# Performance work log

Hardware: AMD Instinct MI355X
Metric: run time of the kernel (lower is better)

Reference implementation:

```python
import jax, jax.numpy as jnp
import numpy as np

HIDDEN_DIM = 256
NLAT, NLON = 64, 128
BATCH, N_STATIONS = 2, 1024


def _grid_coords():
    lat = jnp.linspace(-90.0, 90.0, NLAT)
    lon = jnp.linspace(-180.0, 180.0, NLON)
    lat_mesh, lon_mesh = jnp.meshgrid(lat, lon, indexing='ij')
    return lat_mesh.reshape(-1), lon_mesh.reshape(-1)  # (n_grid,)


def setup_inputs() -> dict:
    key = jax.random.key(0)
    k1, k2, k3, k4, k5, k6 = jax.random.split(key, 6)
    station_features = jax.random.normal(k1, (BATCH, N_STATIONS, HIDDEN_DIM), dtype=jnp.float32)
    station_coords = jax.random.normal(k2, (BATCH, N_STATIONS, 3), dtype=jnp.float32)
    mask = jnp.ones((BATCH, N_STATIONS), dtype=jnp.float32)
    # distance_mlp params: Linear(3,32) -> GELU -> Linear(32,1) -> Softplus
    W1 = jax.random.normal(k3, (3, 32), dtype=jnp.float32) * (1.0 / np.sqrt(3.0))
    b1 = jax.random.normal(k4, (32,), dtype=jnp.float32) * 0.02
    W2 = jax.random.normal(k5, (32, 1), dtype=jnp.float32) * (1.0 / np.sqrt(32.0))
    b2 = jax.random.normal(k6, (1,), dtype=jnp.float32) * 0.02
    return {"station_features": station_features, "station_coords": station_coords,
            "mask": mask, "W1": W1, "b1": b1, "W2": W2, "b2": b2}


def reference(station_features, station_coords, mask, W1, b1, W2, b2):
    lat_grid, lon_grid = _grid_coords()  # (G,)
    station_lat = station_coords[:, :, 0]  # (B,S)
    station_lon = station_coords[:, :, 1]
    dlat = station_lat[:, :, None] - lat_grid[None, None, :]  # (B,S,G)
    dlon = station_lon[:, :, None] - lon_grid[None, None, :]
    dist = jnp.sqrt(dlat**2 + dlon**2 + 1e-6)
    dist_features = jnp.stack([dist, dlat, dlon], axis=-1)  # (B,S,G,3)
    h = jax.nn.gelu(dist_features @ W1 + b1, approximate=False)  # (B,S,G,32)
    weights = jax.nn.softplus((h @ W2 + b2)[..., 0])  # (B,S,G)
    weights = weights * mask[:, :, None]
    weights = jax.nn.softmax(weights, axis=1)  # over stations
    grid = jnp.einsum('bsg,bsd->bgd', weights, station_features)
    grid = grid.reshape(station_features.shape[0], NLAT, NLON, HIDDEN_DIM)
    return jnp.transpose(grid, (0, 3, 1, 2))  # (B, D, nlat, nlon)
```

## Files before the change

kernel.cpp:

```cpp
#include <hip/hip_runtime.h>
#include <math.h>

#define NLAT 64
#define NLON 128
#define HID  256
#define NSTA 1024
#define NG   (NLAT * NLON)
#define TG   16
#define SC   128
#define NCH  4
#define NGRP 16
#define TABN 2048
#define TABW 4.5f

#define LOG2E 1.4426950408889634f
#define LN2   0.69314718055994531f

typedef float f32x4 __attribute__((ext_vector_type(4)));
typedef _Float16 f16x8 __attribute__((ext_vector_type(8)));

__device__ __forceinline__ float gelu_ref(float x) {
    const float p  = 0.3275911f;
    const float a1 = 0.254829592f, a2 = -0.284496736f, a3 = 1.421413741f,
                a4 = -1.453152027f, a5 = 1.061405429f;
    float z  = x * 0.70710678118654752f;
    float az = fabsf(z);
    float t  = __builtin_amdgcn_rcpf(fmaf(p, az, 1.0f));
    float poly = fmaf(fmaf(fmaf(fmaf(a5, t, a4), t, a3), t, a2), t, a1) * t;
    float e  = __builtin_amdgcn_exp2f(az * az * -LOG2E);
    float r  = fmaf(-poly, e, 1.0f);
    float erfz = copysignf(r, z);
    float hx = 0.5f * x;
    return fmaf(hx, erfz, hx);
}

__global__ __launch_bounds__(256)
void cvt_kernel(const float* __restrict__ feats, _Float16* __restrict__ fhi,
                _Float16* __restrict__ flo) {
    __shared__ float tile[32][68];
    const int blk = blockIdx.x;
    const int b  = blk >> 7;
    const int st = (blk >> 2) & 31;
    const int dt = blk & 3;
    {
        const int s  = threadIdx.x >> 3;
        const int dq = threadIdx.x & 7;
        const float* src = feats + ((size_t)(b * NSTA + st * 32 + s)) * HID + dt * 64 + dq * 8;
        float4 v0 = *(const float4*)src;
        float4 v1 = *(const float4*)(src + 4);
        *(float4*)&tile[s][dq * 8]     = v0;
        *(float4*)&tile[s][dq * 8 + 4] = v1;
    }
    __syncthreads();
    const int d  = threadIdx.x >> 2;
    const int sq = threadIdx.x & 3;
    f16x8 hi8, lo8;
#pragma unroll
    for (int k = 0; k < 8; ++k) {
        float v = tile[sq * 8 + k][d];
        _Float16 h = (_Float16)v;
        hi8[k] = h;
        lo8[k] = (_Float16)(v - (float)h);
    }
    const size_t o = ((size_t)(b * HID + dt * 64 + d)) * NSTA + st * 32 + sq * 8;
    *(f16x8*)&fhi[o] = hi8;
    *(f16x8*)&flo[o] = lo8;
}

__global__ __launch_bounds__(256, 6)
void s2g_kernel(const float* __restrict__ coords,
                const float* __restrict__ maskp,
                const float* __restrict__ W1,
                const float* __restrict__ b1,
                const float* __restrict__ W2,
                const float* __restrict__ b2p,
                const _Float16* __restrict__ fhi,
                const _Float16* __restrict__ flo,
                float* __restrict__ out,
                float* __restrict__ acc1,
                float2* __restrict__ ml)
{
    __shared__ float gtab[TABN];
    __shared__ __align__(16) f16x8 fragAh[256];
    __shared__ __align__(16) f16x8 fragAl[256];
    __shared__ __align__(16) float slat[SC], slon[SC], smask[SC];
    __shared__ float4 wpack[32];
    __shared__ float2 w2pk[32];
    __shared__ __align__(16) float redbuf[NGRP * TG];
    __shared__ __align__(16) float mS[TG], lS[TG], alphaS[TG];

    const int tid  = threadIdx.x;
    const int half = blockIdx.x >> 10;
    const int b    = (blockIdx.x >> 9) & 1;
    const int blk  = blockIdx.x & 511;
    const int lat  = blk >> 3;
    const int lon0 = (blk & 7) * TG;
    const int sbase = half * (NSTA / 2);

    const float latv = -90.0f + (180.0f / 63.0f) * (float)lat;

    const float CELL   = TABW / (float)TABN;
    const float ISCALE = (float)TABN / TABW;

#pragma unroll
    for (int k = tid; k < TABN; k += 256) {
        float x = ((float)k + 0.5f) * CELL;
        gtab[k] = gelu_ref(-x);
    }
    if (tid < 32) {
        wpack[tid] = make_float4(W1[tid] * ISCALE, W1[32 + tid] * ISCALE,
                                 W1[64 + tid] * ISCALE, b1[tid] * ISCALE);
        w2pk[tid]  = make_float2(W2[tid], W2[tid] * CELL);
        if (tid < TG) { mS[tid] = -1.0e30f; lS[tid] = 0.0f; }
    }
    const float b2 = b2p[0];

    const int gA   = tid & (TG - 1);
    const int sgrp = tid >> 4;
    const float lonvA = -180.0f + (360.0f / 127.0f) * (float)(lon0 + gA);

    const int lane = tid & 63;
    const int wv   = tid >> 6;

    f32x4 acc[4];
#pragma unroll
    for (int t = 0; t < 4; ++t) acc[t] = (f32x4){0.0f, 0.0f, 0.0f, 0.0f};

    const float* cbase = coords + (size_t)b * NSTA * 3;
    const float* mbase = maskp  + (size_t)b * NSTA;
    const _Float16* fhb = fhi + (size_t)b * HID * NSTA;
    const _Float16* flb = flo + (size_t)b * HID * NSTA;

    for (int c = 0; c < NCH; ++c) {
        const int s0 = sbase + c * SC;
        __syncthreads();
        if (tid < SC) {
            slat[tid]  = cbase[(size_t)(s0 + tid) * 3 + 0];
            slon[tid]  = cbase[(size_t)(s0 + tid) * 3 + 1];
            smask[tid] = mbase[s0 + tid];
        }
        __syncthreads();

        float dist[8], dlat[8], dlon[8], v[8];
#pragma unroll
        for (int i = 0; i < 8; ++i) {
            int s = sgrp * 8 + i;
            float dla = slat[s] - latv;
            float dlo = slon[s] - lonvA;
            dlat[i] = dla;
            dlon[i] = dlo;
            dist[i] = sqrtf(fmaf(dla, dla, fmaf(dlo, dlo, 1e-6f)));
            v[i] = b2;
        }
#pragma unroll 2
        for (int j = 0; j < 32; ++j) {
            float4 wj = wpack[j];
            float2 w2 = w2pk[j];
#pragma unroll
            for (int i = 0; i < 8; ++i) {
                float pre = fmaf(wj.x, dist[i], fmaf(wj.y, dlat[i], fmaf(wj.z, dlon[i], wj.w)));
                float a   = fminf(fabsf(pre), (float)TABN - 0.5f);
                int  idx  = (int)a;
                float r   = gtab[idx];
                v[i] = fmaf(w2.y, fmaxf(pre, 0.0f), v[i]);
                v[i] = fmaf(w2.x, r, v[i]);
            }
        }
        float lmax = -3.0e38f;
#pragma unroll
        for (int i = 0; i < 8; ++i) {
            int s = sgrp * 8 + i;
            float x  = v[i];
            float ax = fabsf(x);
            float e  = __builtin_amdgcn_exp2f(-ax * LOG2E);
            float sp = fmaxf(x, 0.0f) + __builtin_amdgcn_logf(1.0f + e) * LN2;
            v[i] = sp * smask[s];
            lmax = fmaxf(lmax, v[i]);
        }
        redbuf[sgrp * TG + gA] = lmax;
        __syncthreads();

        if (tid < TG) {
            float cm = redbuf[tid];
#pragma unroll
            for (int k = 1; k < NGRP; ++k) cm = fmaxf(cm, redbuf[k * TG + tid]);
            float mold = mS[tid];
            float mnew = fmaxf(mold, cm);
            alphaS[tid] = __builtin_amdgcn_exp2f((mold - mnew) * LOG2E);
            mS[tid] = mnew;
        }
        __syncthreads();

        {
            float m  = mS[gA];
            float ps = 0.0f;
            f16x8 fh, fl;
#pragma unroll
            for (int i = 0; i < 8; ++i) {
                float p = __builtin_amdgcn_exp2f((v[i] - m) * LOG2E);
                _Float16 h = (_Float16)p;
                fh[i] = h;
                fl[i] = (_Float16)(p - (float)h);
                ps += p;
            }
            const int idx = ((sgrp >> 2) << 6) + (((sgrp & 3) << 4) | gA);
            fragAh[idx] = fh;
            fragAl[idx] = fl;
            redbuf[sgrp * TG + gA] = ps;
        }
        __syncthreads();

        if (tid < TG) {
            float t = 0.0f;
#pragma unroll
            for (int k = 0; k < NGRP; ++k) t += redbuf[k * TG + tid];
            lS[tid] = lS[tid] * alphaS[tid] + t;
        }

        {
            const f32x4 al = *(const f32x4*)&alphaS[(lane >> 4) * 4];
#pragma unroll
            for (int t = 0; t < 4; ++t) acc[t] = acc[t] * al;

            const int srow = s0 + ((lane >> 4) * 8);
            const int dbase = wv * 64 + (lane & 15);
#pragma unroll
            for (int kc = 0; kc < 4; ++kc) {
                f16x8 ah = fragAh[(kc << 6) + lane];
                f16x8 al16 = fragAl[(kc << 6) + lane];
#pragma unroll
                for (int t = 0; t < 4; ++t) {
                    const size_t off = (size_t)(dbase + t * 16) * NSTA + srow + kc * 32;
                    f16x8 bh = *(const f16x8*)(fhb + off);
                    f16x8 bl = *(const f16x8*)(flb + off);
                    acc[t] = __builtin_amdgcn_mfma_f32_16x16x32_f16(ah, bh, acc[t], 0, 0, 0);
                    acc[t] = __builtin_amdgcn_mfma_f32_16x16x32_f16(ah, bl, acc[t], 0, 0, 0);
                    acc[t] = __builtin_amdgcn_mfma_f32_16x16x32_f16(al16, bh, acc[t], 0, 0, 0);
                }
            }
        }
    }
    __syncthreads();

    {
        float* dst = half ? acc1 : out;
        const int m0 = (lane >> 4) * 4;
        const size_t gbase = (size_t)lat * NLON + lon0 + m0;
#pragma unroll
        for (int t = 0; t < 4; ++t) {
            const int d = wv * 64 + t * 16 + (lane & 15);
            *reinterpret_cast<f32x4*>(dst + ((size_t)(b * HID + d)) * NG + gbase) = acc[t];
        }
        if (tid < TG)
            ml[((half << 1) + b) * NG + lat * NLON + lon0 + tid] = make_float2(mS[tid], lS[tid]);
    }
}

__global__ __launch_bounds__(256)
void comb_kernel(float* __restrict__ out, const float* __restrict__ acc1,
                 const float2* __restrict__ ml) {
    const int x    = blockIdx.x;
    const int b    = x >> 9;
    const int lat  = (x >> 3) & 63;
    const int dseg = x & 7;
    const int lon  = threadIdx.x & 127;
    const int dsub = threadIdx.x >> 7;
    const int g    = lat * NLON + lon;

    const float2 p0 = ml[b * NG + g];
    const float2 p1 = ml[(2 + b) * NG + g];
    const float M  = fmaxf(p0.x, p1.x);
    float s0 = __builtin_amdgcn_exp2f((p0.x - M) * LOG2E);
    float s1 = __builtin_amdgcn_exp2f((p1.x - M) * LOG2E);
    const float rl = 1.0f / fmaf(p0.y, s0, p1.y * s1);
    s0 *= rl; s1 *= rl;

#pragma unroll 4
    for (int k = 0; k < 16; ++k) {
        const int d = dseg * 32 + dsub + k * 2;
        const size_t o = ((size_t)(b * HID + d)) * NG + g;
        out[o] = fmaf(out[o], s0, acc1[o] * s1);
    }
}

extern "C" void kernel_launch(void* const* d_in, const int* in_sizes, int n_in,
                              void* d_out, int out_size, void* d_ws, size_t ws_size,
                              hipStream_t stream) {
    const float* feats  = (const float*)d_in[0];
    const float* coords = (const float*)d_in[1];
    const float* maskp  = (const float*)d_in[2];
    const float* W1     = (const float*)d_in[3];
    const float* b1     = (const float*)d_in[4];
    const float* W2     = (const float*)d_in[5];
    const float* b2     = (const float*)d_in[6];
    float* out          = (float*)d_out;

    _Float16* fhi = (_Float16*)d_ws;
    _Float16* flo = fhi + (size_t)2 * HID * NSTA;
    float*  acc1 = (float*)((char*)d_ws + (size_t)2 * 1048576);
    float2* ml   = (float2*)((char*)d_ws + (size_t)2 * 1048576 + (size_t)2 * HID * NG * 4);

    hipLaunchKernelGGL(cvt_kernel, dim3(256), dim3(256), 0, stream, feats, fhi, flo);
    hipLaunchKernelGGL(s2g_kernel, dim3(2048), dim3(256), 0, stream,
                       coords, maskp, W1, b1, W2, b2, fhi, flo, out, acc1, ml);
    hipLaunchKernelGGL(comb_kernel, dim3(1024), dim3(256), 0, stream, out, acc1, ml);
}
```

Measured before the change: 255.0 us.

## Fold GELU linear part into per-station term and precompute weights in prep kernel

```diff
diff --git a/kernel.cpp b/kernel.cpp
--- a/kernel.cpp
+++ b/kernel.cpp
@@ -35,10 +35,37 @@
 }
 
 __global__ __launch_bounds__(256)
-void cvt_kernel(const float* __restrict__ feats, _Float16* __restrict__ fhi,
-                _Float16* __restrict__ flo) {
+void cvt_kernel(const float* __restrict__ feats,
+                const float* __restrict__ W1, const float* __restrict__ b1,
+                const float* __restrict__ W2, const float* __restrict__ b2p,
+                _Float16* __restrict__ fhi, _Float16* __restrict__ flo,
+                float* __restrict__ wbuf) {
+    const int blk = blockIdx.x;
+    if (blk == 256) {
+        if (threadIdx.x == 0) {
+            const float ISCALE = (float)TABN / TABW;
+            const float CELL   = TABW / (float)TABN;
+            float A = 0.0f, B = 0.0f, C = 0.0f, D = b2p[0];
+            for (int j = 0; j < 32; ++j) {
+                float a = W1[j], b = W1[32 + j], c = W1[64 + j], d = b1[j], w2 = W2[j];
+                wbuf[j * 8 + 0] = a * ISCALE;
+                wbuf[j * 8 + 1] = b * ISCALE;
+                wbuf[j * 8 + 2] = c * ISCALE;
+                wbuf[j * 8 + 3] = d * ISCALE;
+                wbuf[j * 8 + 4] = w2;
+                wbuf[j * 8 + 5] = 0.5f * w2 * CELL;
+                wbuf[j * 8 + 6] = 0.0f;
+                wbuf[j * 8 + 7] = 0.0f;
+                A = fmaf(0.5f * w2, a, A);
+                B = fmaf(0.5f * w2, b, B);
+                C = fmaf(0.5f * w2, c, C);
+                D = fmaf(0.5f * w2, d, D);
+            }
+            wbuf[256] = A; wbuf[257] = B; wbuf[258] = C; wbuf[259] = D;
+        }
+        return;
+    }
     __shared__ float tile[32][68];
-    const int blk = blockIdx.x;
     const int b  = blk >> 7;
     const int st = (blk >> 2) & 31;
     const int dt = blk & 3;
@@ -70,10 +97,7 @@
 __global__ __launch_bounds__(256, 6)
 void s2g_kernel(const float* __restrict__ coords,
                 const float* __restrict__ maskp,
-                const float* __restrict__ W1,
-                const float* __restrict__ b1,
-                const float* __restrict__ W2,
-                const float* __restrict__ b2p,
+                const float* __restrict__ wbuf,
                 const _Float16* __restrict__ fhi,
                 const _Float16* __restrict__ flo,
                 float* __restrict__ out,
@@ -83,10 +107,8 @@
     __shared__ float gtab[TABN];
     __shared__ __align__(16) f16x8 fragAh[256];
     __shared__ __align__(16) f16x8 fragAl[256];
-    __shared__ __align__(16) float slat[SC], slon[SC], smask[SC];
-    __shared__ float4 wpack[32];
-    __shared__ float2 w2pk[32];
-    __shared__ __align__(16) float redbuf[NGRP * TG];
+    __shared__ __align__(16) float maxbuf[NGRP * TG];
+    __shared__ __align__(16) float psum[NGRP * TG];
     __shared__ __align__(16) float mS[TG], lS[TG], alphaS[TG];
 
     const int tid  = threadIdx.x;
@@ -98,22 +120,17 @@
     const int sbase = half * (NSTA / 2);
 
     const float latv = -90.0f + (180.0f / 63.0f) * (float)lat;
-
-    const float CELL   = TABW / (float)TABN;
-    const float ISCALE = (float)TABN / TABW;
-
+    const float LIM  = (float)TABN - 0.5f;
+
+    const float CELL = TABW / (float)TABN;
 #pragma unroll
     for (int k = tid; k < TABN; k += 256) {
         float x = ((float)k + 0.5f) * CELL;
         gtab[k] = gelu_ref(-x);
     }
-    if (tid < 32) {
-        wpack[tid] = make_float4(W1[tid] * ISCALE, W1[32 + tid] * ISCALE,
-                                 W1[64 + tid] * ISCALE, b1[tid] * ISCALE);
-        w2pk[tid]  = make_float2(W2[tid], W2[tid] * CELL);
-        if (tid < TG) { mS[tid] = -1.0e30f; lS[tid] = 0.0f; }
-    }
-    const float b2 = b2p[0];
+    if (tid < TG) { mS[tid] = -1.0e30f; lS[tid] = 0.0f; }
+
+    const f32x4 lin = *(const f32x4*)&wbuf[256];
 
     const int gA   = tid & (TG - 1);
     const int sgrp = tid >> 4;
@@ -131,59 +148,55 @@
     const _Float16* fhb = fhi + (size_t)b * HID * NSTA;
     const _Float16* flb = flo + (size_t)b * HID * NSTA;
 
+    __syncthreads();
+
     for (int c = 0; c < NCH; ++c) {
         const int s0 = sbase + c * SC;
-        __syncthreads();
-        if (tid < SC) {
-            slat[tid]  = cbase[(size_t)(s0 + tid) * 3 + 0];
-            slon[tid]  = cbase[(size_t)(s0 + tid) * 3 + 1];
-            smask[tid] = mbase[s0 + tid];
-        }
-        __syncthreads();
 
         float dist[8], dlat[8], dlon[8], v[8];
 #pragma unroll
         for (int i = 0; i < 8; ++i) {
-            int s = sgrp * 8 + i;
-            float dla = slat[s] - latv;
-            float dlo = slon[s] - lonvA;
+            const int s = s0 + sgrp * 8 + i;
+            float sla = cbase[(size_t)s * 3 + 0];
+            float slo = cbase[(size_t)s * 3 + 1];
+            float dla = sla - latv;
+            float dlo = slo - lonvA;
             dlat[i] = dla;
             dlon[i] = dlo;
-            dist[i] = sqrtf(fmaf(dla, dla, fmaf(dlo, dlo, 1e-6f)));
-            v[i] = b2;
+            float dss = sqrtf(fmaf(dla, dla, fmaf(dlo, dlo, 1e-6f)));
+            dist[i] = dss;
+            v[i] = fmaf(lin.x, dss, fmaf(lin.y, dla, fmaf(lin.z, dlo, lin.w)));
         }
 #pragma unroll 2
         for (int j = 0; j < 32; ++j) {
-            float4 wj = wpack[j];
-            float2 w2 = w2pk[j];
+            const f32x4 wq = *(const f32x4*)&wbuf[j * 8];
+            const float2 wp = *(const float2*)&wbuf[j * 8 + 4];
 #pragma unroll
             for (int i = 0; i < 8; ++i) {
-                float pre = fmaf(wj.x, dist[i], fmaf(wj.y, dlat[i], fmaf(wj.z, dlon[i], wj.w)));
-                float a   = fminf(fabsf(pre), (float)TABN - 0.5f);
-                int  idx  = (int)a;
-                float r   = gtab[idx];
-                v[i] = fmaf(w2.y, fmaxf(pre, 0.0f), v[i]);
-                v[i] = fmaf(w2.x, r, v[i]);
+                float pre = fmaf(wq.x, dist[i], fmaf(wq.y, dlat[i], fmaf(wq.z, dlon[i], wq.w)));
+                v[i] = fmaf(wp.y, fabsf(pre), v[i]);
+                float a = fminf(fabsf(pre), LIM);
+                v[i] = fmaf(wp.x, gtab[(unsigned)a], v[i]);
             }
         }
         float lmax = -3.0e38f;
 #pragma unroll
         for (int i = 0; i < 8; ++i) {
-            int s = sgrp * 8 + i;
+            const int s = s0 + sgrp * 8 + i;
             float x  = v[i];
             float ax = fabsf(x);
             float e  = __builtin_amdgcn_exp2f(-ax * LOG2E);
             float sp = fmaxf(x, 0.0f) + __builtin_amdgcn_logf(1.0f + e) * LN2;
-            v[i] = sp * smask[s];
+            v[i] = sp * mbase[s];
             lmax = fmaxf(lmax, v[i]);
         }
-        redbuf[sgrp * TG + gA] = lmax;
+        maxbuf[sgrp * TG + gA] = lmax;
         __syncthreads();
 
         if (tid < TG) {
-            float cm = redbuf[tid];
-#pragma unroll
-            for (int k = 1; k < NGRP; ++k) cm = fmaxf(cm, redbuf[k * TG + tid]);
+            float cm = maxbuf[tid];
+#pragma unroll
+            for (int k = 1; k < NGRP; ++k) cm = fmaxf(cm, maxbuf[k * TG + tid]);
             float mold = mS[tid];
             float mnew = fmaxf(mold, cm);
             alphaS[tid] = __builtin_amdgcn_exp2f((mold - mnew) * LOG2E);
@@ -206,14 +219,14 @@
             const int idx = ((sgrp >> 2) << 6) + (((sgrp & 3) << 4) | gA);
             fragAh[idx] = fh;
             fragAl[idx] = fl;
-            redbuf[sgrp * TG + gA] = ps;
+            psum[sgrp * TG + gA] = ps;
         }
         __syncthreads();
 
         if (tid < TG) {
             float t = 0.0f;
 #pragma unroll
-            for (int k = 0; k < NGRP; ++k) t += redbuf[k * TG + tid];
+            for (int k = 0; k < NGRP; ++k) t += psum[k * TG + tid];
             lS[tid] = lS[tid] * alphaS[tid] + t;
         }
 
@@ -299,9 +312,11 @@
     _Float16* flo = fhi + (size_t)2 * HID * NSTA;
     float*  acc1 = (float*)((char*)d_ws + (size_t)2 * 1048576);
     float2* ml   = (float2*)((char*)d_ws + (size_t)2 * 1048576 + (size_t)2 * HID * NG * 4);
-
-    hipLaunchKernelGGL(cvt_kernel, dim3(256), dim3(256), 0, stream, feats, fhi, flo);
+    float*  wbuf = (float*)((char*)d_ws + (size_t)2 * 1048576 + (size_t)2 * HID * NG * 4 + 262144);
+
+    hipLaunchKernelGGL(cvt_kernel, dim3(257), dim3(256), 0, stream,
+                       feats, W1, b1, W2, b2, fhi, flo, wbuf);
     hipLaunchKernelGGL(s2g_kernel, dim3(2048), dim3(256), 0, stream,
-                       coords, maskp, W1, b1, W2, b2, fhi, flo, out, acc1, ml);
+                       coords, maskp, wbuf, fhi, flo, out, acc1, ml);
     hipLaunchKernelGGL(comb_kernel, dim3(1024), dim3(256), 0, stream, out, acc1, ml);
 }
```

Result: slower. 271.0 us (+6.2%).
